# Kernel tuning notes

Measured on AMD Instinct MI355X. Metric: run time of the kernel, lower is better.

Reference implementation:

```python
import jax, jax.numpy as jnp
import numpy as np

N_NODES = 100000


def _gcn_norm(edge_index, num_nodes):
    # PyG gcn_norm with add_self_loops=True, edge_weight=1:
    # A_hat = A + I; norm_e = deg^{-1/2}[src] * deg^{-1/2}[dst]
    loop = jnp.arange(num_nodes, dtype=edge_index.dtype)
    src = jnp.concatenate([edge_index[0], loop])
    dst = jnp.concatenate([edge_index[1], loop])
    deg = jax.ops.segment_sum(jnp.ones_like(src, dtype=jnp.float32), dst,
                              num_segments=num_nodes)
    dinv = jnp.where(deg > 0, jax.lax.rsqrt(deg), 0.0)
    norm = dinv[src] * dinv[dst]  # [E + N]
    return src, dst, norm


def _gcn_conv(x, src, dst, norm, W, b, num_nodes):
    h = x @ W                                  # [N, out] dense GEMM
    msg = h[src] * norm[:, None]               # gather + scale per edge
    out = jax.ops.segment_sum(msg, dst, num_segments=num_nodes)
    return out + b


def setup_inputs() -> dict:
    key = jax.random.key(0)
    k1, k2, k3, k4, k5, k6 = jax.random.split(key, 6)
    in_c, hid_c, out_c = 128, 128, 64
    E = 3200000
    x = jax.random.normal(k1, (N_NODES, in_c), dtype=jnp.float32)
    edge_index = jax.random.randint(k2, (2, E), 0, N_NODES, dtype=jnp.int64)
    # Glorot-style init for GCNConv linear weights, zero bias (PyG default)
    W1 = jax.random.normal(k3, (in_c, hid_c), dtype=jnp.float32) / np.sqrt(in_c)
    b1 = jnp.zeros((hid_c,), dtype=jnp.float32)
    W2 = jax.random.normal(k4, (hid_c, out_c), dtype=jnp.float32) / np.sqrt(hid_c)
    b2 = jnp.zeros((out_c,), dtype=jnp.float32)
    return {"x": x, "edge_index": edge_index, "W1": W1, "b1": b1,
            "W2": W2, "b2": b2}


def reference(x, edge_index, W1, b1, W2, b2):
    # Dropout is identity in eval mode (F.dropout(training=False)).
    src, dst, norm = _gcn_norm(edge_index, N_NODES)
    h = _gcn_conv(x, src, dst, norm, W1, b1, N_NODES)
    out = _gcn_conv(h, src, dst, norm, W2, b2, N_NODES)
    return out
```

## Files before the change

kernel.cpp:

```cpp
#include <hip/hip_runtime.h>
#include <hip/hip_fp16.h>
#include <cstdint>
#include <cstddef>


#define NB    391
#define BSH   8
#define CAPS  32
#define PBLK  512
#define OVB   64
#define CAPB  9216

typedef _Float16 half8 __attribute__((ext_vector_type(8)));
typedef float    floatx4 __attribute__((ext_vector_type(4)));
typedef unsigned uint4v  __attribute__((ext_vector_type(4)));


__global__ __launch_bounds__(256) void partition_k(
    const int* __restrict__ src, const int* __restrict__ dst,
    int* __restrict__ cursor, unsigned long long* __restrict__ ov64,
    int* __restrict__ ovcnt, int* __restrict__ csr, int E) {
    __shared__ unsigned stag[NB][CAPS + 1];
    __shared__ int scnt[NB];
    __shared__ int sbase[NB];
    __shared__ int ovn;
    const int t = threadIdx.x, bid = blockIdx.x;
    for (int i = t; i < NB; i += 256) scnt[i] = 0;
    if (t == 0) ovn = 0;
    __syncthreads();

    const int Q = E >> 2;
    const int per = (Q + PBLK - 1) / PBLK;
    const int qbeg = bid * per;
    const int qend = min(qbeg + per, Q);
    const int4* src4 = (const int4*)src;
    const int4* dst4 = (const int4*)dst;

    for (int q = qbeg + t; q < qend; q += 256) {
        const int4 s4 = src4[q];
        const int4 d4 = dst4[q];
#pragma unroll
        for (int j = 0; j < 4; ++j) {
            const int s = (&s4.x)[j], d = (&d4.x)[j];
            const int b = d >> BSH;
            const unsigned rec = ((unsigned)(d & 255) << 17) | (unsigned)s;
            const int slot = atomicAdd(&scnt[b], 1);
            if (slot < CAPS) stag[b][slot] = rec;
            else {
                const int pos = atomicAdd(&ovn, 1);
                if (pos < OVB)
                    ov64[(size_t)bid * OVB + pos] =
                        ((unsigned long long)(unsigned)d << 17) | (unsigned)s;
            }
        }
    }
    if (bid == 0) {
        for (int e = (E & ~3) + t; e < E; e += 256) {
            const int s = src[e], d = dst[e];
            const int b = d >> BSH;
            const unsigned rec = ((unsigned)(d & 255) << 17) | (unsigned)s;
            const int slot = atomicAdd(&scnt[b], 1);
            if (slot < CAPS) stag[b][slot] = rec;
            else {
                const int pos = atomicAdd(&ovn, 1);
                if (pos < OVB)
                    ov64[(size_t)bid * OVB + pos] =
                        ((unsigned long long)(unsigned)d << 17) | (unsigned)s;
            }
        }
    }
    __syncthreads();

    for (int b = t; b < NB; b += 256)
        sbase[b] = atomicAdd(&cursor[b], min(scnt[b], CAPS));
    __syncthreads();

    for (int i = t; i < NB * CAPS; i += 256) {
        const int b = i >> 5, j = i & 31;
        if (j < min(scnt[b], CAPS))
            csr[(size_t)b * CAPB + sbase[b] + j] = (int)stag[b][j];
    }
    if (t == 0) ovcnt[bid] = min(ovn, OVB);
}

__global__ __launch_bounds__(256) void build_w12_k(
    const int* __restrict__ cursor,
    const unsigned long long* __restrict__ ov64, const int* __restrict__ ovcnt,
    int* __restrict__ rbeg, int* __restrict__ rend,
    int* __restrict__ csr, float* __restrict__ dinv,
    const float* __restrict__ W1, const float* __restrict__ W2,
    const float* __restrict__ b1, _Float16* __restrict__ BhiT,
    _Float16* __restrict__ BloT, float* __restrict__ c2, int N) {
    __shared__ unsigned lrec[CAPB + 64];
    __shared__ int cnt[256];
    __shared__ int scan[256];
    __shared__ int lpos[256];
    __shared__ int ovn_sh;
    const int t = threadIdx.x, b = blockIdx.x;

    if (b >= NB) {
        const int bb = b - NB;
        if (bb < 32) {
            const int r = bb * 4 + (t >> 6);
            const int c = t & 63;
            float acc = 0.f;
            for (int k = 0; k < 128; ++k) acc += W1[r * 128 + k] * W2[k * 64 + c];
            const _Float16 h = (_Float16)acc;
            BhiT[c * 128 + r] = h;
            BloT[c * 128 + r] = (_Float16)(acc - (float)h);
        } else if (t < 64) {
            float acc = 0.f;
            for (int k = 0; k < 128; ++k) acc += b1[k] * W2[k * 64 + t];
            c2[t] = acc;
        }
        return;
    }

    const int n0 = b << BSH;
    const int nn = min(256, N - n0);
    const int gbase = b * CAPB;
    const int tstag = cursor[b];

    cnt[t] = 0;
    if (t == 0) ovn_sh = 0;
    __syncthreads();

    for (int i = t; i < tstag; i += 256) lrec[i] = (unsigned)csr[gbase + i];
    for (int blk = t; blk < PBLK; blk += 256) {
        const int c = ovcnt[blk];
        for (int i2 = 0; i2 < c; ++i2) {
            const unsigned long long r = ov64[(size_t)blk * OVB + i2];
            const int dd = (int)(r >> 17);
            if ((dd >> BSH) == b) {
                const int pos = atomicAdd(&ovn_sh, 1);
                lrec[tstag + pos] =
                    ((unsigned)(dd & 255) << 17) | (unsigned)(r & 0x1FFFFu);
            }
        }
    }
    __syncthreads();

    const int tot = tstag + ovn_sh;
    for (int i = t; i < tot; i += 256) atomicAdd(&cnt[lrec[i] >> 17], 1);
    __syncthreads();

    scan[t] = cnt[t];
    __syncthreads();
    for (int o = 1; o < 256; o <<= 1) {
        int x = (t >= o) ? scan[t - o] : 0;
        __syncthreads(); scan[t] += x; __syncthreads();
    }
    const int excl = scan[t] - cnt[t];
    lpos[t] = excl;
    if (t < nn) {
        rbeg[n0 + t] = gbase + excl;
        rend[n0 + t] = gbase + scan[t];
        dinv[n0 + t] = rsqrtf((float)(cnt[t] + 1));
    }
    __syncthreads();

    for (int i = t; i < tot; i += 256) {
        const unsigned r = lrec[i];
        const int pq = atomicAdd(&lpos[r >> 17], 1);
        csr[gbase + pq] = (int)(r & 0x1FFFFu);
    }
}

__global__ __launch_bounds__(256) void gemm_mfma_k(
    const float* __restrict__ X, const _Float16* __restrict__ BhiT,
    const _Float16* __restrict__ BloT, const float* __restrict__ dinv,
    __half* __restrict__ g, int N) {
    const int t = threadIdx.x;
    const int wave = t >> 6, lane = t & 63;
    const int m16 = lane & 15;
    const int quad = lane >> 4;
    const int rowbase = blockIdx.x * 64 + wave * 16;
    const int arow = min(rowbase + m16, N - 1);

    floatx4 acc[4] = {{0.f,0.f,0.f,0.f},{0.f,0.f,0.f,0.f},
                      {0.f,0.f,0.f,0.f},{0.f,0.f,0.f,0.f}};

#pragma unroll
    for (int ks = 0; ks < 4; ++ks) {
        const int k0 = ks * 32 + quad * 8;
        const float4 xa = *(const float4*)(X + (size_t)arow * 128 + k0);
        const float4 xb = *(const float4*)(X + (size_t)arow * 128 + k0 + 4);
        const float xs[8] = {xa.x, xa.y, xa.z, xa.w, xb.x, xb.y, xb.z, xb.w};
        half8 ahi, alo;
#pragma unroll
        for (int j = 0; j < 8; ++j) {
            const _Float16 h = (_Float16)xs[j];
            ahi[j] = h;
            alo[j] = (_Float16)(xs[j] - (float)h);
        }
#pragma unroll
        for (int c = 0; c < 4; ++c) {
            const int n = c * 16 + m16;
            const half8 bhi = *(const half8*)(BhiT + n * 128 + k0);
            const half8 blo = *(const half8*)(BloT + n * 128 + k0);
            acc[c] = __builtin_amdgcn_mfma_f32_16x16x32_f16(ahi, bhi, acc[c], 0, 0, 0);
            acc[c] = __builtin_amdgcn_mfma_f32_16x16x32_f16(ahi, blo, acc[c], 0, 0, 0);
            acc[c] = __builtin_amdgcn_mfma_f32_16x16x32_f16(alo, bhi, acc[c], 0, 0, 0);
        }
    }

#pragma unroll
    for (int r = 0; r < 4; ++r) {
        const int grow = rowbase + quad * 4 + r;
        if (grow < N) {
            const float di = dinv[grow];
#pragma unroll
            for (int c = 0; c < 4; ++c)
                g[(size_t)grow * 64 + c * 16 + m16] = __float2half(acc[c][r] * di);
        }
    }
}

template <int PASS2>
__global__ __launch_bounds__(256) void agg_k(
    const __half* __restrict__ gin, const int* __restrict__ rbeg,
    const int* __restrict__ rend, const int* __restrict__ csr,
    const float* __restrict__ dinv, void* __restrict__ outp,
    float* __restrict__ p, const float* __restrict__ c2,
    const float* __restrict__ b2, int N) {
    const int wv = (blockIdx.x * 256 + threadIdx.x) >> 6;
    const int lane = threadIdx.x & 63;
    const int half = lane >> 5;
    const int d = wv * 2 + half;
    if (d >= N) return;
    const int w    = lane & 7;
    const int slot = (lane >> 3) & 3;
    const int beg = rbeg[d], end = rend[d];
    const float di = dinv[d];
    const half8* __restrict__ grow = (const half8*)gin;

    const half8 vself = grow[((size_t)d << 3) + w];

    float acc[8];
#pragma unroll
    for (int q = 0; q < 8; ++q) acc[q] = 0.f;
    float accp = (!PASS2 && slot == 0) ? di : 0.f;

    auto accum = [&](half8 f) {
        const uint4v u = __builtin_bit_cast(uint4v, f);
#pragma unroll
        for (int q = 0; q < 4; ++q) {
            asm("v_fma_mix_f32 %0, %1, 1.0, %0 op_sel:[0,0,0] op_sel_hi:[1,0,0]"
                : "+v"(acc[2 * q]) : "v"(u[q]));
            asm("v_fma_mix_f32 %0, %1, 1.0, %0 op_sel:[1,0,0] op_sel_hi:[1,0,0]"
                : "+v"(acc[2 * q + 1]) : "v"(u[q]));
        }
    };

    int e = beg + slot;
    while (e + 12 < end) {
        const int s0 = csr[e], s1 = csr[e + 4], s2 = csr[e + 8], s3 = csr[e + 12];
        const half8 f0 = grow[((size_t)s0 << 3) + w];
        const half8 f1 = grow[((size_t)s1 << 3) + w];
        const half8 f2 = grow[((size_t)s2 << 3) + w];
        const half8 f3 = grow[((size_t)s3 << 3) + w];
        if (!PASS2) accp += dinv[s0] + dinv[s1] + dinv[s2] + dinv[s3];
        accum(f0); accum(f1); accum(f2); accum(f3);
        e += 16;
    }
    if (e + 4 < end) {
        const int s0 = csr[e], s1 = csr[e + 4];
        const half8 f0 = grow[((size_t)s0 << 3) + w];
        const half8 f1 = grow[((size_t)s1 << 3) + w];
        if (!PASS2) accp += dinv[s0] + dinv[s1];
        accum(f0); accum(f1);
        e += 8;
    }
    while (e < end) {
        const int s0 = csr[e];
        const half8 f0 = grow[((size_t)s0 << 3) + w];
        if (!PASS2) accp += dinv[s0];
        accum(f0);
        e += 4;
    }

#pragma unroll
    for (int m = 8; m <= 16; m <<= 1) {
#pragma unroll
        for (int q = 0; q < 8; ++q) acc[q] += __shfl_xor(acc[q], m);
        if (!PASS2) accp += __shfl_xor(accp, m);
    }

    if (slot == 0) {
        const __half2* sh2 = (const __half2*)&vself;
#pragma unroll
        for (int q = 0; q < 4; ++q) {
            const float2 t2 = __half22float2(sh2[q]);
            acc[2 * q]     += t2.x;
            acc[2 * q + 1] += t2.y;
        }
        if (PASS2) {
            const float pd = p[d];
            float o[8];
#pragma unroll
            for (int q = 0; q < 8; ++q)
                o[q] = acc[q] * di + pd * c2[w * 8 + q] + b2[w * 8 + q];
            float4* op = (float4*)outp + ((size_t)d << 4) + w * 2;
            op[0] = make_float4(o[0], o[1], o[2], o[3]);
            op[1] = make_float4(o[4], o[5], o[6], o[7]);
        } else {
            const float sc = di * di;
            half8 ov;
#pragma unroll
            for (int q = 0; q < 8; ++q) ov[q] = (_Float16)(acc[q] * sc);
            ((half8*)outp)[((size_t)d << 3) + w] = ov;
            if ((lane & 31) == 0) p[d] = di * accp;
        }
    }
}

extern "C" void kernel_launch(void* const* d_in, const int* in_sizes, int n_in,
                              void* d_out, int out_size, void* d_ws, size_t ws_size,
                              hipStream_t stream) {
    const float* x  = (const float*)d_in[0];
    const int*   ei = (const int*)d_in[1];
    const float* W1 = (const float*)d_in[2];
    const float* b1 = (const float*)d_in[3];
    const float* W2 = (const float*)d_in[4];
    const float* b2 = (const float*)d_in[5];
    float* out = (float*)d_out;

    const int N = in_sizes[0] / 128;
    const int E = in_sizes[1] / 2;
    const int* src = ei;
    const int* dst = ei + E;

    char* ws = (char*)d_ws;
    auto take = [&](size_t bytes) { char* q = ws; ws += (bytes + 255) & ~(size_t)255; return q; };
    int*      cursor  = (int*)     take((size_t)NB * 4);
    int*      rbeg    = (int*)     take((size_t)N * 4);
    int*      rendp   = (int*)     take((size_t)N * 4);
    float*    dinv    = (float*)   take((size_t)N * 4);
    float*    pbuf    = (float*)   take((size_t)N * 4);
    _Float16* BhiT    = (_Float16*)take(128 * 64 * 2);
    _Float16* BloT    = (_Float16*)take(128 * 64 * 2);
    float*    c2      = (float*)   take(64 * 4);
    int*      ovcnt   = (int*)     take((size_t)PBLK * 4);
    unsigned long long* ov64 = (unsigned long long*)take((size_t)PBLK * OVB * 8);
    int*      csr     = (int*)     take((size_t)NB * CAPB * 4);
    __half*   g       = (__half*)  take((size_t)N * 64 * 2);
    __half*   t1      = (__half*)  take((size_t)N * 64 * 2);

    hipMemsetAsync(cursor, 0, (size_t)NB * 4, stream);

    partition_k<<<PBLK, 256, 0, stream>>>(src, dst, cursor, ov64, ovcnt, csr, E);
    build_w12_k<<<NB + 33, 256, 0, stream>>>(cursor, ov64, ovcnt,
                                             rbeg, rendp, csr, dinv,
                                             W1, W2, b1, BhiT, BloT, c2, N);
    gemm_mfma_k<<<(N + 63) / 64, 256, 0, stream>>>(x, BhiT, BloT, dinv, g, N);

    const int aggBlocks = (N + 7) / 8;
    agg_k<0><<<aggBlocks, 256, 0, stream>>>(g,  rbeg, rendp, csr, dinv, t1,  pbuf, c2, b2, N);
    agg_k<1><<<aggBlocks, 256, 0, stream>>>(t1, rbeg, rendp, csr, dinv, out, pbuf, c2, b2, N);
}
```

Before: 285.0 us.

## Fuse weight precompute into partition and GEMM into CSR build kernel

Moves the W1·W2 and b1·W2 precompute blocks into the partition kernel, and runs the MFMA GEMM as extra blocks of the CSR build kernel. This removes one kernel launch and lets the GEMM overlap with the CSR build. Because the GEMM no longer knows dinv, it writes unscaled output. The first aggregation pass now scales each gathered neighbor by dinv[src] through a v_fma_mix multiply and scales the self term by dinv[d]. That adds per-edge arithmetic to the aggregation, and the build kernel becomes heavier in LDS use, which may reduce how many GEMM blocks run at once.

```diff
diff --git a/kernel.cpp b/kernel.cpp
--- a/kernel.cpp
+++ b/kernel.cpp
@@ -16,15 +16,37 @@
 typedef unsigned uint4v  __attribute__((ext_vector_type(4)));
 
 
-__global__ __launch_bounds__(256) void partition_k(
+__global__ __launch_bounds__(256) void part_w12_k(
     const int* __restrict__ src, const int* __restrict__ dst,
     int* __restrict__ cursor, unsigned long long* __restrict__ ov64,
-    int* __restrict__ ovcnt, int* __restrict__ csr, int E) {
+    int* __restrict__ ovcnt, int* __restrict__ csr,
+    const float* __restrict__ W1, const float* __restrict__ W2,
+    const float* __restrict__ b1, _Float16* __restrict__ BhiT,
+    _Float16* __restrict__ BloT, float* __restrict__ c2, int E) {
     __shared__ unsigned stag[NB][CAPS + 1];
     __shared__ int scnt[NB];
     __shared__ int sbase[NB];
     __shared__ int ovn;
     const int t = threadIdx.x, bid = blockIdx.x;
+
+    if (bid >= PBLK) {
+        const int bb = bid - PBLK;
+        if (bb < 32) {
+            const int r = bb * 4 + (t >> 6);
+            const int c = t & 63;
+            float acc = 0.f;
+            for (int k = 0; k < 128; ++k) acc += W1[r * 128 + k] * W2[k * 64 + c];
+            const _Float16 h = (_Float16)acc;
+            BhiT[c * 128 + r] = h;
+            BloT[c * 128 + r] = (_Float16)(acc - (float)h);
+        } else if (t < 64) {
+            float acc = 0.f;
+            for (int k = 0; k < 128; ++k) acc += b1[k] * W2[k * 64 + t];
+            c2[t] = acc;
+        }
+        return;
+    }
+
     for (int i = t; i < NB; i += 256) scnt[i] = 0;
     if (t == 0) ovn = 0;
     __syncthreads();
@@ -83,14 +105,13 @@
     if (t == 0) ovcnt[bid] = min(ovn, OVB);
 }
 
-__global__ __launch_bounds__(256) void build_w12_k(
+__global__ __launch_bounds__(256) void build_gemm_k(
     const int* __restrict__ cursor,
     const unsigned long long* __restrict__ ov64, const int* __restrict__ ovcnt,
     int* __restrict__ rbeg, int* __restrict__ rend,
     int* __restrict__ csr, float* __restrict__ dinv,
-    const float* __restrict__ W1, const float* __restrict__ W2,
-    const float* __restrict__ b1, _Float16* __restrict__ BhiT,
-    _Float16* __restrict__ BloT, float* __restrict__ c2, int N) {
+    const float* __restrict__ X, const _Float16* __restrict__ BhiT,
+    const _Float16* __restrict__ BloT, __half* __restrict__ g, int N) {
     __shared__ unsigned lrec[CAPB + 64];
     __shared__ int cnt[256];
     __shared__ int scan[256];
@@ -99,19 +120,48 @@
     const int t = threadIdx.x, b = blockIdx.x;
 
     if (b >= NB) {
-        const int bb = b - NB;
-        if (bb < 32) {
-            const int r = bb * 4 + (t >> 6);
-            const int c = t & 63;
-            float acc = 0.f;
-            for (int k = 0; k < 128; ++k) acc += W1[r * 128 + k] * W2[k * 64 + c];
-            const _Float16 h = (_Float16)acc;
-            BhiT[c * 128 + r] = h;
-            BloT[c * 128 + r] = (_Float16)(acc - (float)h);
-        } else if (t < 64) {
-            float acc = 0.f;
-            for (int k = 0; k < 128; ++k) acc += b1[k] * W2[k * 64 + t];
-            c2[t] = acc;
+        const int gb = b - NB;
+        const int wave = t >> 6, lane = t & 63;
+        const int m16 = lane & 15;
+        const int quad = lane >> 4;
+        const int rowbase = gb * 64 + wave * 16;
+        const int arow = min(rowbase + m16, N - 1);
+
+        floatx4 acc[4] = {{0.f,0.f,0.f,0.f},{0.f,0.f,0.f,0.f},
+                          {0.f,0.f,0.f,0.f},{0.f,0.f,0.f,0.f}};
+
+#pragma unroll
+        for (int ks = 0; ks < 4; ++ks) {
+            const int k0 = ks * 32 + quad * 8;
+            const float4 xa = *(const float4*)(X + (size_t)arow * 128 + k0);
+            const float4 xb = *(const float4*)(X + (size_t)arow * 128 + k0 + 4);
+            const float xs[8] = {xa.x, xa.y, xa.z, xa.w, xb.x, xb.y, xb.z, xb.w};
+            half8 ahi, alo;
+#pragma unroll
+            for (int j = 0; j < 8; ++j) {
+                const _Float16 h = (_Float16)xs[j];
+                ahi[j] = h;
+                alo[j] = (_Float16)(xs[j] - (float)h);
+            }
+#pragma unroll
+            for (int c = 0; c < 4; ++c) {
+                const int n = c * 16 + m16;
+                const half8 bhi = *(const half8*)(BhiT + n * 128 + k0);
+                const half8 blo = *(const half8*)(BloT + n * 128 + k0);
+                acc[c] = __builtin_amdgcn_mfma_f32_16x16x32_f16(ahi, bhi, acc[c], 0, 0, 0);
+                acc[c] = __builtin_amdgcn_mfma_f32_16x16x32_f16(ahi, blo, acc[c], 0, 0, 0);
+                acc[c] = __builtin_amdgcn_mfma_f32_16x16x32_f16(alo, bhi, acc[c], 0, 0, 0);
+            }
+        }
+
+#pragma unroll
+        for (int r = 0; r < 4; ++r) {
+            const int grow = rowbase + quad * 4 + r;
+            if (grow < N) {
+#pragma unroll
+                for (int c = 0; c < 4; ++c)
+                    g[(size_t)grow * 64 + c * 16 + m16] = __float2half(acc[c][r]);
+            }
         }
         return;
     }
@@ -163,56 +213,6 @@
         const unsigned r = lrec[i];
         const int pq = atomicAdd(&lpos[r >> 17], 1);
         csr[gbase + pq] = (int)(r & 0x1FFFFu);
-    }
-}
-
-__global__ __launch_bounds__(256) void gemm_mfma_k(
-    const float* __restrict__ X, const _Float16* __restrict__ BhiT,
-    const _Float16* __restrict__ BloT, const float* __restrict__ dinv,
-    __half* __restrict__ g, int N) {
-    const int t = threadIdx.x;
-    const int wave = t >> 6, lane = t & 63;
-    const int m16 = lane & 15;
-    const int quad = lane >> 4;
-    const int rowbase = blockIdx.x * 64 + wave * 16;
-    const int arow = min(rowbase + m16, N - 1);
-
-    floatx4 acc[4] = {{0.f,0.f,0.f,0.f},{0.f,0.f,0.f,0.f},
-                      {0.f,0.f,0.f,0.f},{0.f,0.f,0.f,0.f}};
-
-#pragma unroll
-    for (int ks = 0; ks < 4; ++ks) {
-        const int k0 = ks * 32 + quad * 8;
-        const float4 xa = *(const float4*)(X + (size_t)arow * 128 + k0);
-        const float4 xb = *(const float4*)(X + (size_t)arow * 128 + k0 + 4);
-        const float xs[8] = {xa.x, xa.y, xa.z, xa.w, xb.x, xb.y, xb.z, xb.w};
-        half8 ahi, alo;
-#pragma unroll
-        for (int j = 0; j < 8; ++j) {
-            const _Float16 h = (_Float16)xs[j];
-            ahi[j] = h;
-            alo[j] = (_Float16)(xs[j] - (float)h);
-        }
-#pragma unroll
-        for (int c = 0; c < 4; ++c) {
-            const int n = c * 16 + m16;
-            const half8 bhi = *(const half8*)(BhiT + n * 128 + k0);
-            const half8 blo = *(const half8*)(BloT + n * 128 + k0);
-            acc[c] = __builtin_amdgcn_mfma_f32_16x16x32_f16(ahi, bhi, acc[c], 0, 0, 0);
-            acc[c] = __builtin_amdgcn_mfma_f32_16x16x32_f16(ahi, blo, acc[c], 0, 0, 0);
-            acc[c] = __builtin_amdgcn_mfma_f32_16x16x32_f16(alo, bhi, acc[c], 0, 0, 0);
-        }
-    }
-
-#pragma unroll
-    for (int r = 0; r < 4; ++r) {
-        const int grow = rowbase + quad * 4 + r;
-        if (grow < N) {
-            const float di = dinv[grow];
-#pragma unroll
-            for (int c = 0; c < 4; ++c)
-                g[(size_t)grow * 64 + c * 16 + m16] = __float2half(acc[c][r] * di);
-        }
     }
 }
 
@@ -241,14 +241,21 @@
     for (int q = 0; q < 8; ++q) acc[q] = 0.f;
     float accp = (!PASS2 && slot == 0) ? di : 0.f;
 
-    auto accum = [&](half8 f) {
+    auto accum = [&](half8 f, float ds) {
         const uint4v u = __builtin_bit_cast(uint4v, f);
 #pragma unroll
         for (int q = 0; q < 4; ++q) {
-            asm("v_fma_mix_f32 %0, %1, 1.0, %0 op_sel:[0,0,0] op_sel_hi:[1,0,0]"
-                : "+v"(acc[2 * q]) : "v"(u[q]));
-            asm("v_fma_mix_f32 %0, %1, 1.0, %0 op_sel:[1,0,0] op_sel_hi:[1,0,0]"
-                : "+v"(acc[2 * q + 1]) : "v"(u[q]));
+            if (PASS2) {
+                asm("v_fma_mix_f32 %0, %1, 1.0, %0 op_sel:[0,0,0] op_sel_hi:[1,0,0]"
+                    : "+v"(acc[2 * q]) : "v"(u[q]));
+                asm("v_fma_mix_f32 %0, %1, 1.0, %0 op_sel:[1,0,0] op_sel_hi:[1,0,0]"
+                    : "+v"(acc[2 * q + 1]) : "v"(u[q]));
+            } else {
+                asm("v_fma_mix_f32 %0, %1, %2, %0 op_sel:[0,0,0] op_sel_hi:[1,0,0]"
+                    : "+v"(acc[2 * q]) : "v"(u[q]), "v"(ds));
+                asm("v_fma_mix_f32 %0, %1, %2, %0 op_sel:[1,0,0] op_sel_hi:[1,0,0]"
+                    : "+v"(acc[2 * q + 1]) : "v"(u[q]), "v"(ds));
+            }
         }
     };
 
@@ -259,23 +266,29 @@
         const half8 f1 = grow[((size_t)s1 << 3) + w];
         const half8 f2 = grow[((size_t)s2 << 3) + w];
         const half8 f3 = grow[((size_t)s3 << 3) + w];
-        if (!PASS2) accp += dinv[s0] + dinv[s1] + dinv[s2] + dinv[s3];
-        accum(f0); accum(f1); accum(f2); accum(f3);
+        float d0 = 0.f, d1 = 0.f, d2 = 0.f, d3 = 0.f;
+        if (!PASS2) {
+            d0 = dinv[s0]; d1 = dinv[s1]; d2 = dinv[s2]; d3 = dinv[s3];
+            accp += d0 + d1 + d2 + d3;
+        }
+        accum(f0, d0); accum(f1, d1); accum(f2, d2); accum(f3, d3);
         e += 16;
     }
     if (e + 4 < end) {
         const int s0 = csr[e], s1 = csr[e + 4];
         const half8 f0 = grow[((size_t)s0 << 3) + w];
         const half8 f1 = grow[((size_t)s1 << 3) + w];
-        if (!PASS2) accp += dinv[s0] + dinv[s1];
-        accum(f0); accum(f1);
+        float d0 = 0.f, d1 = 0.f;
+        if (!PASS2) { d0 = dinv[s0]; d1 = dinv[s1]; accp += d0 + d1; }
+        accum(f0, d0); accum(f1, d1);
         e += 8;
     }
     while (e < end) {
         const int s0 = csr[e];
         const half8 f0 = grow[((size_t)s0 << 3) + w];
-        if (!PASS2) accp += dinv[s0];
-        accum(f0);
+        float d0 = 0.f;
+        if (!PASS2) { d0 = dinv[s0]; accp += d0; }
+        accum(f0, d0);
         e += 4;
     }
 
@@ -291,8 +304,13 @@
 #pragma unroll
         for (int q = 0; q < 4; ++q) {
             const float2 t2 = __half22float2(sh2[q]);
-            acc[2 * q]     += t2.x;
-            acc[2 * q + 1] += t2.y;
+            if (PASS2) {
+                acc[2 * q]     += t2.x;
+                acc[2 * q + 1] += t2.y;
+            } else {
+                acc[2 * q]     += t2.x * di;
+                acc[2 * q + 1] += t2.y * di;
+            }
         }
         if (PASS2) {
             const float pd = p[d];
@@ -348,11 +366,13 @@
 
     hipMemsetAsync(cursor, 0, (size_t)NB * 4, stream);
 
-    partition_k<<<PBLK, 256, 0, stream>>>(src, dst, cursor, ov64, ovcnt, csr, E);
-    build_w12_k<<<NB + 33, 256, 0, stream>>>(cursor, ov64, ovcnt,
-                                             rbeg, rendp, csr, dinv,
-                                             W1, W2, b1, BhiT, BloT, c2, N);
-    gemm_mfma_k<<<(N + 63) / 64, 256, 0, stream>>>(x, BhiT, BloT, dinv, g, N);
+    part_w12_k<<<PBLK + 33, 256, 0, stream>>>(src, dst, cursor, ov64, ovcnt, csr,
+                                              W1, W2, b1, BhiT, BloT, c2, E);
+
+    const int gemmBlocks = (N + 63) / 64;
+    build_gemm_k<<<NB + gemmBlocks, 256, 0, stream>>>(cursor, ov64, ovcnt,
+                                                      rbeg, rendp, csr, dinv,
+                                                      x, BhiT, BloT, g, N);
 
     const int aggBlocks = (N + 7) / 8;
     agg_k<0><<<aggBlocks, 256, 0, stream>>>(g,  rbeg, rendp, csr, dinv, t1,  pbuf, c2, b2, N);
```

Measured after the change: 279.1 us. 2.1% less time.
